# Performance work log

Hardware: AMD Instinct MI355X
Metric: run time of the kernel (lower is better)

Reference implementation:

```python
import jax, jax.numpy as jnp
import numpy as np

B, X, Y, Z = 2, 64, 64, 48
T_IN, T_OUT = 10, 20
WIDTH = 20
G = 4              # number of fields / groups
M1 = M2 = M3 = 8   # fourier modes
L = 4              # layers
ORDER = [[0, 1, 2, 3], [1, 2, 3, 0], [2, 3, 0, 1], [3, 0, 1, 2]]
CIN = WIDTH * 4    # mWidth_input_parameters[i] == 4
COUT = WIDTH       # nWidth_output_parameters[i] == 1
EPS = 1e-5


def setup_inputs() -> dict:
    key = jax.random.key(0)
    ks = jax.random.split(key, 12)
    s = 0.02
    return {
        "x": jax.random.normal(ks[0], (B, X, Y, Z, G * T_IN), jnp.float32),
        "p_w": jax.random.normal(ks[1], (G, T_IN + 3, WIDTH), jnp.float32) * s,
        "p_b": jnp.zeros((G, WIDTH), jnp.float32),
        # complex spectral weights stored as (..., 2) = (real, imag); 4 corner blocks
        "spec_w": jax.random.normal(ks[2], (L, G, 4, CIN, COUT, M1, M2, M3, 2), jnp.float32) * (1.0 / CIN),
        "mlp_w1": jax.random.normal(ks[3], (L, G, COUT, COUT), jnp.float32) * s,
        "mlp_b1": jnp.zeros((L, G, COUT), jnp.float32),
        "mlp_w2": jax.random.normal(ks[4], (L, G, COUT, COUT), jnp.float32) * s,
        "mlp_b2": jnp.zeros((L, G, COUT), jnp.float32),
        "w_w": jax.random.normal(ks[5], (L, G, COUT, CIN), jnp.float32) * s,
        "w_b": jnp.zeros((L, G, COUT), jnp.float32),
        "q_w1": jax.random.normal(ks[6], (G, 4 * COUT, COUT), jnp.float32) * s,
        "q_b1": jnp.zeros((G, 4 * COUT), jnp.float32),
        "q_w2": jax.random.normal(ks[7], (G, T_OUT, 4 * COUT), jnp.float32) * s,
        "q_b2": jnp.zeros((G, T_OUT), jnp.float32),
    }


def _instance_norm(v):  # (B,C,X,Y,Z); InstanceNorm3d, affine=False
    m = v.mean(axis=(-3, -2, -1), keepdims=True)
    var = v.var(axis=(-3, -2, -1), keepdims=True)
    return (v - m) * jax.lax.rsqrt(var + EPS)


def _conv1x1(v, w, b):  # w: (Co, Ci)
    return jnp.einsum('bixyz,oi->boxyz', v, w) + b[None, :, None, None, None]


def _gelu(v):
    return jax.nn.gelu(v, approximate=False)


def _spectral(v, w):  # v: (B,Ci,X,Y,Z); w: complex (4,Ci,Co,M1,M2,M3)
    ft = jnp.fft.rfftn(v, axes=(-3, -2, -1))
    mul = lambda xc, wc: jnp.einsum('bixyz,ioxyz->boxyz', xc, wc)
    out = jnp.zeros((v.shape[0], w.shape[2], X, Y, Z // 2 + 1), ft.dtype)
    out = out.at[:, :, :M1, :M2, :M3].set(mul(ft[:, :, :M1, :M2, :M3], w[0]))
    out = out.at[:, :, -M1:, :M2, :M3].set(mul(ft[:, :, -M1:, :M2, :M3], w[1]))
    out = out.at[:, :, :M1, -M2:, :M3].set(mul(ft[:, :, :M1, -M2:, :M3], w[2]))
    out = out.at[:, :, -M1:, -M2:, :M3].set(mul(ft[:, :, -M1:, -M2:, :M3], w[3]))
    return jnp.fft.irfftn(out, s=(X, Y, Z), axes=(-3, -2, -1))


def _grid():  # (1,X,Y,Z,3), linspace 0..1 per axis
    gx = jnp.linspace(0.0, 1.0, X, dtype=jnp.float32)[:, None, None]
    gy = jnp.linspace(0.0, 1.0, Y, dtype=jnp.float32)[None, :, None]
    gz = jnp.linspace(0.0, 1.0, Z, dtype=jnp.float32)[None, None, :]
    g = jnp.stack([jnp.broadcast_to(gx, (X, Y, Z)),
                   jnp.broadcast_to(gy, (X, Y, Z)),
                   jnp.broadcast_to(gz, (X, Y, Z))], axis=-1)
    return g[None]


def reference(x, p_w, p_b, spec_w, mlp_w1, mlp_b1, mlp_w2, mlp_b2,
              w_w, w_b, q_w1, q_b1, q_w2, q_b2):
    grid = jnp.broadcast_to(_grid(), (x.shape[0], X, Y, Z, 3))
    # --- lifting: per-field Linear(T_in+3 -> width) ---
    lifted = [jnp.concatenate([x[..., i * T_IN:(i + 1) * T_IN], grid], axis=-1) @ p_w[i] + p_b[i]
              for i in range(G)]
    h = jnp.concatenate(lifted, axis=-1).transpose(0, 4, 1, 2, 3)  # (B, width*G, X, Y, Z)
    sw = spec_w[..., 0] + 1j * spec_w[..., 1]
    for l in range(L):
        for i in range(G):
            # faithful gather quirk: first index duplicated, last index dropped
            idx = [ORDER[i][0]] + ORDER[i][:-1]
            xg = jnp.concatenate([h[:, WIDTH * k:WIDTH * (k + 1)] for k in idx], axis=1)
            v = _instance_norm(xg)
            v = _spectral(v, sw[l, i])
            v = _instance_norm(v)
            v = _conv1x1(_gelu(_conv1x1(v, mlp_w1[l, i], mlp_b1[l, i])), mlp_w2[l, i], mlp_b2[l, i])
            r = _conv1x1(xg, w_w[l, i], w_b[l, i])
            h = h.at[:, WIDTH * i:WIDTH * (i + 1)].set(v + r)
        if l != L - 1:
            h = _gelu(h)
    # --- projection: per-field MLP (T_OUT == WIDTH so slices align to field blocks) ---
    outs = []
    for i in range(G):
        lo = (WIDTH if i == 0 else T_OUT) * i
        xi = h[:, lo:lo + WIDTH]
        xi = _conv1x1(_gelu(_conv1x1(xi, q_w1[i], q_b1[i])), q_w2[i], q_b2[i])
        outs.append(xi)
    out = jnp.concatenate(outs, axis=1)
    return out.transpose(0, 2, 3, 4, 1)  # (B,X,Y,Z,G*T_OUT)
```

## Files before the change

kernel.cpp:

```cpp
#include <hip/hip_runtime.h>
#include <math.h>

#define SPAT 196608
#define EPSV 1e-5f

__device__ __forceinline__ float geluf(float x){
    return 0.5f*x*(1.0f + erff(x*0.70710678118654752440f));
}
__device__ __forceinline__ float wred(float v){
    #pragma unroll
    for(int o=32;o>0;o>>=1) v += __shfl_down(v,o);
    return v;
}

__global__ void k_tables(float* tab){
    for(int idx=threadIdx.x; idx<384; idx+=blockDim.x){
        int z = idx>>3, k = idx&7;
        double a = 6.283185307179586476925286766559 * (double)((k*z)%48) / 48.0;
        float c = (float)cos(a), s = (float)sin(a);
        tab[idx]=c; tab[384+idx]=s;
        tab[768 + k*48+z]=c; tab[1152 + k*48+z]=s;
    }
    for(int idx=threadIdx.x; idx<1024; idx+=blockDim.x){
        int y = idx>>4, ki = idx&15;
        int ka = ki<8 ? ki : ki+48;
        double a = 6.283185307179586476925286766559 * (double)((ka*y)%64) / 64.0;
        float c=(float)cos(a), s=(float)sin(a);
        tab[1536+idx]=c; tab[2560+idx]=s;
        tab[3584 + ki*64+y]=c; tab[4608 + ki*64+y]=s;
    }
}

__global__ void __launch_bounds__(256) k_lift(const float* __restrict__ x,
                       const float* __restrict__ pw, const float* __restrict__ pb,
                       float* __restrict__ h){
    int t = blockIdx.x*256 + threadIdx.x;
    int b = (t>=SPAT) ? 1 : 0; int col = t - b*SPAT;
    int xy = col/48, z = col%48;
    const float4* xp = (const float4*)(x + (size_t)t*40);
    float in[40];
    #pragma unroll
    for(int q=0;q<10;q++){
        float4 v = xp[q];
        in[q*4]=v.x; in[q*4+1]=v.y; in[q*4+2]=v.z; in[q*4+3]=v.w;
    }
    float gx = (float)(xy>>6)*(1.0f/63.0f);
    float gy = (float)(xy&63)*(1.0f/63.0f);
    float gz = (float)z*(1.0f/47.0f);
    for(int g=0;g<4;g++){
        const float* w = pw + g*260;
        #pragma unroll 4
        for(int c=0;c<20;c++){
            float a = pb[g*20+c];
            #pragma unroll
            for(int j=0;j<10;j++) a += in[g*10+j]*w[j*20+c];
            a += gx*w[200+c] + gy*w[220+c] + gz*w[240+c];
            h[(size_t)(b*80+g*20+c)*SPAT + col] = a;
        }
    }
}

__global__ void __launch_bounds__(256) k_zy(const float* __restrict__ h,
        float* __restrict__ ybuf, float* __restrict__ partZY,
        const float* __restrict__ tab, int gA,int gB,int gC,int gD){
    __shared__ __align__(16) float hl[64*52];
    __shared__ float sp[16*65];
    __shared__ float cyl[16*65], syl[16*65];
    __shared__ float sred[8];
    int blk = blockIdx.x;
    int x = blk&63; int d=(blk>>6)%20; int r2 = blk/1280; int b = r2&1; int gi = r2>>1;
    int gl4[4]={gA,gB,gC,gD};
    int g = gl4[gi];
    int ch = g*20+d;
    int tid=threadIdx.x;
    const float4* src = (const float4*)(h + (size_t)(b*80+ch)*SPAT + (size_t)x*3072);
    float s1=0,s2=0;
    #pragma unroll
    for(int u=0;u<3;u++){
        int e=tid+u*256; float4 v=src[e];
        int y=e/12, zq=e%12;
        *(float4*)(hl + y*52 + zq*4) = v;
        s1 += v.x+v.y+v.z+v.w; s2 += v.x*v.x+v.y*v.y+v.z*v.z+v.w*v.w;
    }
    for(int tt=tid;tt<1024;tt+=256){
        int ki=tt>>6, y=tt&63;
        cyl[ki*65+y]=tab[3584+tt]; syl[ki*65+y]=tab[4608+tt];
    }
    s1=wred(s1); s2=wred(s2);
    if((tid&63)==0){ sred[(tid>>6)*2]=s1; sred[(tid>>6)*2+1]=s2; }
    __syncthreads();
    if(tid==0){
        size_t pi = ((size_t)(b*80+ch)*64+x)*2;
        partZY[pi]   = sred[0]+sred[2]+sred[4]+sred[6];
        partZY[pi+1] = sred[1]+sred[3]+sred[5]+sred[7];
    }
    {
        int y = tid&63; int kq = tid>>6;
        float v[48];
        const float4* hr4 = (const float4*)(hl + y*52);
        #pragma unroll
        for(int q=0;q<12;q++){
            float4 t4=hr4[q];
            v[q*4]=t4.x; v[q*4+1]=t4.y; v[q*4+2]=t4.z; v[q*4+3]=t4.w;
        }
        #pragma unroll
        for(int kk=0;kk<2;kk++){
            int k = kq*2+kk;
            const float* CZ = tab+768+k*48;
            const float* SZ = tab+1152+k*48;
            float rr=0, si=0;
            #pragma unroll
            for(int z=0;z<48;z++){ rr += v[z]*CZ[z]; si += v[z]*SZ[z]; }
            sp[(k*2)*65+y]=rr; sp[(k*2+1)*65+y]=-si;
        }
    }
    __syncthreads();
    if(tid<128){
        int ky=tid>>3, kz=tid&7;
        const float* cy = cyl+ky*65; const float* sy = syl+ky*65;
        const float* spr = sp + (kz*2)*65;
        const float* spi = sp + (kz*2+1)*65;
        float fr=0, fi=0;
        #pragma unroll 8
        for(int y=0;y<64;y++){
            float sr=spr[y], si=spi[y];
            float c=cy[y], s=sy[y];
            fr += sr*c + si*s;
            fi += si*c - sr*s;
        }
        size_t base = ((size_t)((g*2+b)*20+d)*16 + ky)*1024 + (size_t)(kz*128);
        ybuf[base + x]      = fr;
        ybuf[base + 64 + x] = fi;
    }
}

__global__ void __launch_bounds__(128) k_xdft(const float* __restrict__ ybuf,
        float* __restrict__ fbufC, const float* __restrict__ partZY,
        const float* __restrict__ tab, int gA,int gB,int gC,int gD){
    __shared__ __align__(16) float ylx[16*68];
    __shared__ float cxl[16*65], sxl[16*65];
    __shared__ float scs[1];
    int blk = blockIdx.x;
    int kyi = blk&15; int d=(blk>>4)%20; int r2=blk/320; int b=r2&1; int gi=r2>>1;
    int gl4[4]={gA,gB,gC,gD};
    int g=gl4[gi]; int ch=g*20+d;
    int tid=threadIdx.x;
    const float4* src = (const float4*)(ybuf + (((size_t)((g*2+b)*20+d)*16+kyi)*1024));
    #pragma unroll
    for(int u=0;u<2;u++){
        int e=tid+u*128; float4 v=src[e];
        int kzri = e>>4; int xx=(e&15)*4;
        *(float4*)(ylx + kzri*68 + xx) = v;
    }
    for(int tt=tid;tt<1024;tt+=128){
        int ki=tt>>6, y=tt&63;
        cxl[ki*65+y]=tab[3584+tt]; sxl[ki*65+y]=tab[4608+tt];
    }
    float s1=0,s2=0;
    if(tid<64){
        size_t pi=((size_t)(b*80+ch)*64+tid)*2;
        s1=partZY[pi]; s2=partZY[pi+1];
    }
    s1=wred(s1); s2=wred(s2);
    if(tid==0){
        float mean=s1*(1.0f/196608.0f);
        float var=s2*(1.0f/196608.0f)-mean*mean;
        scs[0]=rsqrtf(var+EPSV);
    }
    __syncthreads();
    float sc = scs[0];
    int kxi=tid>>3, kz=tid&7;
    const float* yr = ylx + (kz*2)*68;
    const float* yi = ylx + (kz*2+1)*68;
    const float* cx = cxl + kxi*65;
    const float* sx = sxl + kxi*65;
    float fr=0, fi=0;
    #pragma unroll 8
    for(int xx=0;xx<64;xx++){
        float a=yr[xx], e2=yi[xx];
        float c=cx[xx], s=sx[xx];
        fr += a*c + e2*s;
        fi += e2*c - a*s;
    }
    fr*=sc; fi*=sc;
    if(kxi==0 && kyi==0 && kz==0){ fr=0.0f; fi=0.0f; }
    size_t idx = ((size_t)(b*80+ch)*2048 + (size_t)((kxi*16+kyi)*8+kz))*2;
    fbufC[idx]=fr; fbufC[idx+1]=fi;
}

__global__ void __launch_bounds__(256) k_spec(const float* __restrict__ fbufC,
        const float* __restrict__ sw, float* __restrict__ gbuf,
        float* __restrict__ stat2, int li, int g0, int g1, int g2){
    __shared__ float part[2112];
    int blk = blockIdx.x;
    int m1p = blk & 3, o = (blk>>2)%20, q = blk/80;
    int tid = threadIdx.x;
    int t64 = tid & 63, cc = tid >> 6;
    if(q==0 && m1p==0 && tid<2){
        stat2[(tid*20+o)*2]=0.f; stat2[(tid*20+o)*2+1]=0.f;
    }
    int offx = (q&1)*8, offy = (q>>1)*8;
    int m1 = m1p*2 + (t64>>5);
    int m2 = (t64>>2)&7;
    int m3 = (t64&3)*2;
    int tw = m1*64 + m2*8 + m3;
    int kxi = m1+offx, kyi = m2+offy;
    int fo = (kxi*16 + kyi)*8 + m3;
    const float4* wp = (const float4*)(sw + (((size_t)(li*4+q)*1600) + o)*1024 + (size_t)tw*2);
    const float4* fb = (const float4*)fbufC + (fo>>1);
    float r00=0,i00=0,r01=0,i01=0, r10=0,i10=0,r11=0,i11=0;
    int c0 = cc*5;
    #pragma unroll
    for(int u=0;u<5;u++){
        int c = c0+u;
        float4 wa = wp[(size_t)c*5120];
        float4 wb4= wp[(size_t)(c+20)*5120];
        float wr0 = wa.x + wb4.x, wi0 = wa.y + wb4.y, wr1 = wa.z + wb4.z, wi1 = wa.w + wb4.w;
        float4 f0 = fb[(size_t)(g0*20+c)*1024];
        float4 f1 = fb[(size_t)(80+g0*20+c)*1024];
        r00 += f0.x*wr0 - f0.y*wi0; i00 += f0.x*wi0 + f0.y*wr0;
        r01 += f0.z*wr1 - f0.w*wi1; i01 += f0.z*wi1 + f0.w*wr1;
        r10 += f1.x*wr0 - f1.y*wi0; i10 += f1.x*wi0 + f1.y*wr0;
        r11 += f1.z*wr1 - f1.w*wi1; i11 += f1.z*wi1 + f1.w*wr1;
    }
    #pragma unroll
    for(int u=0;u<5;u++){
        int c = c0+u;
        float4 wa = wp[(size_t)(c+40)*5120];
        float4 f0 = fb[(size_t)(g1*20+c)*1024];
        float4 f1 = fb[(size_t)(80+g1*20+c)*1024];
        r00 += f0.x*wa.x - f0.y*wa.y; i00 += f0.x*wa.y + f0.y*wa.x;
        r01 += f0.z*wa.z - f0.w*wa.w; i01 += f0.z*wa.w + f0.w*wa.z;
        r10 += f1.x*wa.x - f1.y*wa.y; i10 += f1.x*wa.y + f1.y*wa.x;
        r11 += f1.z*wa.z - f1.w*wa.w; i11 += f1.z*wa.w + f1.w*wa.z;
    }
    #pragma unroll
    for(int u=0;u<5;u++){
        int c = c0+u;
        float4 wa = wp[(size_t)(c+60)*5120];
        float4 f0 = fb[(size_t)(g2*20+c)*1024];
        float4 f1 = fb[(size_t)(80+g2*20+c)*1024];
        r00 += f0.x*wa.x - f0.y*wa.y; i00 += f0.x*wa.y + f0.y*wa.x;
        r01 += f0.z*wa.z - f0.w*wa.w; i01 += f0.z*wa.w + f0.w*wa.z;
        r10 += f1.x*wa.x - f1.y*wa.y; i10 += f1.x*wa.y + f1.y*wa.x;
        r11 += f1.z*wa.z - f1.w*wa.w; i11 += f1.z*wa.w + f1.w*wa.z;
    }
    float vals[8]={r00,i00,r01,i01,r10,i10,r11,i11};
    #pragma unroll
    for(int e=0;e<8;e++) part[t64*33 + e*4 + cc] = vals[e];
    __syncthreads();
    if(cc==0){
        float acc[8];
        #pragma unroll
        for(int e=0;e<8;e++){
            const float* p = part + t64*33 + e*4;
            acc[e] = p[0]+p[1]+p[2]+p[3];
        }
        float4* gg0 = (float4*)(gbuf + (size_t)o*4096 + fo*2);
        float4* gg1 = (float4*)(gbuf + (size_t)(20+o)*4096 + fo*2);
        *gg0 = make_float4(acc[0],acc[1],acc[2],acc[3]);
        *gg1 = make_float4(acc[4],acc[5],acc[6],acc[7]);
    }
}

__global__ void k_inv(const float* __restrict__ gbuf, float* __restrict__ iybuf,
                      float* __restrict__ stat2, const float* __restrict__ tab){
    __shared__ __align__(16) float gl[4096];
    __shared__ float tmp[256];
    __shared__ float cl[1088], sl[1088];
    __shared__ float ig[4];
    int blk = blockIdx.x;
    int nx = blk&63, o = (blk>>6)%20, b = blk/1280;
    const float4* src4 = (const float4*)(gbuf + (size_t)(b*20+o)*4096);
    for(int t=threadIdx.x;t<1024;t+=blockDim.x) ((float4*)gl)[t]=src4[t];
    for(int t=threadIdx.x;t<1024;t+=blockDim.x){
        int y=t>>4, ki=t&15;
        cl[y*17+ki]=tab[1536+t]; sl[y*17+ki]=tab[2560+t];
    }
    __syncthreads();
    {
        int kyi = threadIdx.x>>3, kz = threadIdx.x&7;
        float ar=0, ai=0;
        #pragma unroll 4
        for(int kxi=0;kxi<16;kxi++){
            float gr = gl[((kxi*16+kyi)*8+kz)*2], gi2 = gl[((kxi*16+kyi)*8+kz)*2+1];
            float c = cl[nx*17+kxi], s = sl[nx*17+kxi];
            ar += gr*c - gi2*s;
            ai += gi2*c + gr*s;
        }
        tmp[threadIdx.x*2]   = ar*(1.0f/64.0f);
        tmp[threadIdx.x*2+1] = ai*(1.0f/64.0f);
    }
    __syncthreads();
    float p1=0,p2=0;
    for(int j=0;j<4;j++){
        int out = threadIdx.x + j*128;
        int ny = out>>3, kz = out&7;
        float ar=0, ai=0;
        #pragma unroll 4
        for(int kyi=0;kyi<16;kyi++){
            float vr = tmp[(kyi*8+kz)*2], vi = tmp[(kyi*8+kz)*2+1];
            float c = cl[ny*17+kyi], s = sl[ny*17+kyi];
            ar += vr*c - vi*s;
            ai += vi*c + vr*s;
        }
        ar *= (1.0f/64.0f); ai *= (1.0f/64.0f);
        size_t idx = ((((size_t)(b*20+o)*64+nx)*64+ny)*8+kz)*2;
        iybuf[idx]=ar; iybuf[idx+1]=ai;
        if(kz==0){ p1 += ar; p2 += ar*ar; }
        else p2 += 2.0f*(ar*ar+ai*ai);
    }
    p2 *= (1.0f/48.0f);
    float r1=wred(p1), r2=wred(p2);
    int wv = threadIdx.x>>6;
    if((threadIdx.x&63)==0){ ig[wv*2]=r1; ig[wv*2+1]=r2; }
    __syncthreads();
    if(threadIdx.x==0){
        atomicAdd(&stat2[(b*20+o)*2],   ig[0]+ig[2]);
        atomicAdd(&stat2[(b*20+o)*2+1], ig[1]+ig[3]);
    }
}

__global__ void __launch_bounds__(256) k_passD(
        const float* __restrict__ iybuf,
        const float* __restrict__ w1, const float* __restrict__ b1,
        const float* __restrict__ w2, const float* __restrict__ b2,
        const float* __restrict__ ww, const float* __restrict__ wb,
        float* __restrict__ h,
        const float* __restrict__ stat2, const float* __restrict__ tab,
        int li, int grp, int g1, int g2){
    __shared__ __align__(16) float dl[2560];
    __shared__ __align__(16) float vl[20*392];
    __shared__ float m2l[20], s2l[20];
    __shared__ float czl[384], szl[384];
    int blk = blockIdx.x;
    int nyt = blk&7, nx=(blk>>3)&63, b = blk>>9;
    int tid = threadIdx.x;
    for(int u=tid; u<640; u+=256){
        int o = u>>5, j = u&31;
        const float4* s4 = (const float4*)(iybuf + ((((size_t)(b*20+o)*64+nx)*64 + nyt*8)*16));
        ((float4*)dl)[o*32+j] = s4[j];
    }
    if(tid<20){
        float S1 = stat2[(b*20+tid)*2], S2 = stat2[(b*20+tid)*2+1];
        float mean = S1*(1.0f/196608.0f);
        float var = S2*(1.0f/196608.0f) - mean*mean;
        m2l[tid]=mean; s2l[tid]=rsqrtf(var+EPSV);
    }
    for(int t=tid;t<384;t+=256){ czl[t]=tab[768+t]; szl[t]=tab[1152+t]; }
    __syncthreads();
    for(int idx=tid; idx<7680; idx+=256){
        int o = idx/384, p = idx%384;
        int ny = p/48, nz = p%48;
        const float* dd = dl + o*128 + ny*16;
        float acc = dd[0];
        #pragma unroll
        for(int k=1;k<8;k++)
            acc += 2.0f*(dd[k*2]*czl[k*48+nz] - dd[k*2+1]*szl[k*48+nz]);
        float xv = acc*(1.0f/48.0f);
        vl[o*392+p] = (xv - m2l[o])*s2l[o];
    }
    __syncthreads();
    const float* W1 = w1 + li*400;
    const float* W2 = w2 + li*400;
    const float* B1 = b1 + li*20;
    const float* B2 = b2 + li*20;
    for(int p=tid; p<384; p+=256){
        float vj[20], t1[20];
        #pragma unroll
        for(int j2=0;j2<20;j2++) vj[j2]=vl[j2*392+p];
        #pragma unroll
        for(int oo=0;oo<20;oo++){
            float a = B1[oo];
            #pragma unroll
            for(int j2=0;j2<20;j2++) a += vj[j2]*W1[oo*20+j2];
            t1[oo] = geluf(a);
        }
        #pragma unroll
        for(int oo=0;oo<20;oo++){
            float a = B2[oo];
            #pragma unroll
            for(int j2=0;j2<20;j2++) a += t1[j2]*W2[oo*20+j2];
            vl[oo*392+p] = a;
        }
    }
    __syncthreads();
    int sb = (nx*64 + nyt*8)*48;
    if(tid<192){
        const float* W = ww + li*1600;
        float2 acc[20];
        #pragma unroll
        for(int o=0;o<20;o++){ float bv = wb[li*20+o]; acc[o].x=bv; acc[o].y=bv; }
        const float* hb = h + (size_t)(b*80)*SPAT + sb + tid*2;
        for(int c=0;c<20;c++){
            float2 v = *(const float2*)(hb + (size_t)(grp*20+c)*SPAT);
            #pragma unroll
            for(int o=0;o<20;o++){
                float w = W[o*80+c] + W[o*80+20+c];
                acc[o].x += w*v.x; acc[o].y += w*v.y;
            }
        }
        for(int c=0;c<20;c++){
            float2 v = *(const float2*)(hb + (size_t)(g1*20+c)*SPAT);
            #pragma unroll
            for(int o=0;o<20;o++){
                float w = W[o*80+40+c];
                acc[o].x += w*v.x; acc[o].y += w*v.y;
            }
        }
        for(int c=0;c<20;c++){
            float2 v = *(const float2*)(hb + (size_t)(g2*20+c)*SPAT);
            #pragma unroll
            for(int o=0;o<20;o++){
                float w = W[o*80+60+c];
                acc[o].x += w*v.x; acc[o].y += w*v.y;
            }
        }
        #pragma unroll
        for(int o=0;o<20;o++){
            float2 mv = *(const float2*)(vl + o*392 + tid*2);
            float2 r; r.x = mv.x + acc[o].x; r.y = mv.y + acc[o].y;
            *(float2*)(h + (size_t)(b*80+grp*20+o)*SPAT + sb + tid*2) = r;
        }
    }
}

__global__ void k_gelu(float* __restrict__ h){
    int blk = blockIdx.x;
    size_t base = (size_t)blk*4096;
    float4* hp = (float4*)(h+base);
    for(int e=threadIdx.x;e<1024;e+=blockDim.x){
        float4 v = hp[e];
        v.x=geluf(v.x); v.y=geluf(v.y); v.z=geluf(v.z); v.w=geluf(v.w);
        hp[e]=v;
    }
}

__global__ void __launch_bounds__(256) k_head(const float* __restrict__ h,
        const float* __restrict__ qw1, const float* __restrict__ qb1,
        const float* __restrict__ qw2, const float* __restrict__ qb2,
        float* __restrict__ out){
    int g = blockIdx.x & 3;
    int t = (blockIdx.x>>2)*256 + threadIdx.x;
    if(t >= 196608) return;
    int b = (t>=98304) ? 1 : 0; int col = (t - b*98304)*2;
    const float* hb = h + (size_t)(b*80+g*20)*SPAT + col;
    float2 in20[20];
    #pragma unroll
    for(int j=0;j<20;j++) in20[j] = *(const float2*)(hb + (size_t)j*SPAT);
    float2 o20[20];
    #pragma unroll
    for(int o2=0;o2<20;o2++){ float bv = qb2[g*20+o2]; o20[o2].x=bv; o20[o2].y=bv; }
    for(int o8=0;o8<80;o8++){
        float bv = qb1[g*80+o8];
        float a0 = bv, a1 = bv;
        #pragma unroll
        for(int j=0;j<20;j++){
            float w = qw1[g*1600 + o8*20 + j];
            a0 += in20[j].x*w; a1 += in20[j].y*w;
        }
        a0 = geluf(a0); a1 = geluf(a1);
        #pragma unroll
        for(int o2=0;o2<20;o2++){
            float w = qw2[g*1600 + o2*80 + o8];
            o20[o2].x += a0*w; o20[o2].y += a1*w;
        }
    }
    float* op0 = out + ((size_t)(b*SPAT)+col)*80 + g*20;
    float* op1 = op0 + 80;
    #pragma unroll
    for(int q2=0;q2<5;q2++){
        *(float4*)(op0 + q2*4) = make_float4(o20[q2*4].x,o20[q2*4+1].x,o20[q2*4+2].x,o20[q2*4+3].x);
        *(float4*)(op1 + q2*4) = make_float4(o20[q2*4].y,o20[q2*4+1].y,o20[q2*4+2].y,o20[q2*4+3].y);
    }
}

extern "C" void kernel_launch(void* const* d_in, const int* in_sizes, int n_in,
                              void* d_out, int out_size, void* d_ws, size_t ws_size,
                              hipStream_t stream){
    (void)in_sizes; (void)n_in; (void)out_size;
    const float* x    = (const float*)d_in[0];
    const float* p_w  = (const float*)d_in[1];
    const float* p_b  = (const float*)d_in[2];
    const float* spec = (const float*)d_in[3];
    const float* w1   = (const float*)d_in[4];
    const float* b1   = (const float*)d_in[5];
    const float* w2   = (const float*)d_in[6];
    const float* b2   = (const float*)d_in[7];
    const float* ww   = (const float*)d_in[8];
    const float* wb   = (const float*)d_in[9];
    const float* qw1  = (const float*)d_in[10];
    const float* qb1  = (const float*)d_in[11];
    const float* qw2  = (const float*)d_in[12];
    const float* qb2  = (const float*)d_in[13];
    float* out = (float*)d_out;
    float* ws  = (float*)d_ws;

    if(ws_size < (size_t)37545552*4) return;

    float* h      = ws;
    float* ybuf   = ws + 31457280;
    float* gbuf   = ws + 34078720;
    float* iyb    = ws + 34242560;
    float* fbufC  = ws + 36864000;
    float* partZY = ws + 37519360;
    float* stat2  = ws + 37539840;
    float* tab    = ws + 37539920;

    k_tables<<<1,256,0,stream>>>(tab);
    k_lift<<<1536,256,0,stream>>>(x, p_w, p_b, h);

    static const int ORD3[4][3] = {{0,1,2},{1,2,3},{2,3,0},{3,0,1}};
    for(int l=0;l<4;l++){
        for(int bi=0;bi<2;bi++){
            if(bi==0){
                k_zy  <<<10240,256,0,stream>>>(h, ybuf, partZY, tab, 0,1,2,3);
                k_xdft<<< 2560,128,0,stream>>>(ybuf, fbufC, partZY, tab, 0,1,2,3);
            } else {
                k_zy  <<< 5120,256,0,stream>>>(h, ybuf, partZY, tab, 0,1,0,0);
                k_xdft<<< 1280,128,0,stream>>>(ybuf, fbufC, partZY, tab, 0,1,0,0);
            }
            for(int ii=0;ii<2;ii++){
                int i = bi*2+ii; int li = l*4+i;
                int g0=ORD3[i][0], g1=ORD3[i][1], g2=ORD3[i][2];
                (void)g0;
                k_spec <<< 320,256,0,stream>>>(fbufC, spec, gbuf, stat2, li, g0,g1,g2);
                k_inv  <<<2560,128,0,stream>>>(gbuf, iyb, stat2, tab);
                k_passD<<<1024,256,0,stream>>>(iyb, w1, b1, w2, b2, ww, wb, h, stat2, tab, li, i, g1, g2);
            }
        }
        if(l<3) k_gelu<<<7680,256,0,stream>>>(h);
    }
    k_head<<<3072,256,0,stream>>>(h, qw1, qb1, qw2, qb2, out);
}
```

Measured before the change: 3.379 ms.

## Fuse inter-layer GELU into consumers, use fast erf, and keep passD in registers

Removes the standalone GELU pass over the hidden state between layers. Instead, GELU is applied lazily wherever the not-yet-updated hidden state is read: in the z/y DFT kernel and in the residual 1x1 conv of passD, controlled by per-group flags. The z/y DFT kernel now loads its row slice straight into registers and reduces partial z-DFTs in shared memory, instead of staging the whole tile. passD computes inverse-z, the MLP and the residual conv per thread in registers, without a shared-memory round trip. GELU now uses an Abramowitz–Stegun erf polynomial with a hardware reciprocal, which trades a little accuracy for fewer instructions.

```diff
diff --git a/kernel.cpp b/kernel.cpp
--- a/kernel.cpp
+++ b/kernel.cpp
@@ -5,7 +5,12 @@
 #define EPSV 1e-5f
 
 __device__ __forceinline__ float geluf(float x){
-    return 0.5f*x*(1.0f + erff(x*0.70710678118654752440f));
+    float ax = fabsf(x)*0.70710678118654752440f;
+    float t = __builtin_amdgcn_rcpf(1.0f + 0.3275911f*ax);
+    float p = ((((1.061405429f*t - 1.453152027f)*t + 1.421413741f)*t - 0.284496736f)*t + 0.254829592f)*t;
+    float e = 1.0f - p*__expf(-ax*ax);
+    float er = copysignf(e, x);
+    return 0.5f*x*(1.0f + er);
 }
 __device__ __forceinline__ float wred(float v){
     #pragma unroll
@@ -62,9 +67,8 @@
 
 __global__ void __launch_bounds__(256) k_zy(const float* __restrict__ h,
         float* __restrict__ ybuf, float* __restrict__ partZY,
-        const float* __restrict__ tab, int gA,int gB,int gC,int gD){
-    __shared__ __align__(16) float hl[64*52];
-    __shared__ float sp[16*65];
+        const float* __restrict__ tab, int gA,int gB,int gC,int gD, int gflag){
+    __shared__ float sp4[4*16*65];
     __shared__ float cyl[16*65], syl[16*65];
     __shared__ float sred[8];
     int blk = blockIdx.x;
@@ -73,18 +77,35 @@
     int g = gl4[gi];
     int ch = g*20+d;
     int tid=threadIdx.x;
-    const float4* src = (const float4*)(h + (size_t)(b*80+ch)*SPAT + (size_t)x*3072);
+    int y = tid&63, q4 = tid>>6;
+    const float4* src = (const float4*)(h + (size_t)(b*80+ch)*SPAT + (size_t)x*3072
+                                          + (size_t)(y*48 + q4*12));
+    float v[12];
+    #pragma unroll
+    for(int u=0;u<3;u++){
+        float4 t4 = src[u];
+        v[u*4]=t4.x; v[u*4+1]=t4.y; v[u*4+2]=t4.z; v[u*4+3]=t4.w;
+    }
+    if(gflag){
+        #pragma unroll
+        for(int j=0;j<12;j++) v[j]=geluf(v[j]);
+    }
     float s1=0,s2=0;
     #pragma unroll
-    for(int u=0;u<3;u++){
-        int e=tid+u*256; float4 v=src[e];
-        int y=e/12, zq=e%12;
-        *(float4*)(hl + y*52 + zq*4) = v;
-        s1 += v.x+v.y+v.z+v.w; s2 += v.x*v.x+v.y*v.y+v.z*v.z+v.w*v.w;
-    }
+    for(int j=0;j<12;j++){ s1+=v[j]; s2+=v[j]*v[j]; }
     for(int tt=tid;tt<1024;tt+=256){
-        int ki=tt>>6, y=tt&63;
-        cyl[ki*65+y]=tab[3584+tt]; syl[ki*65+y]=tab[4608+tt];
+        int ki=tt>>6, yy=tt&63;
+        cyl[ki*65+yy]=tab[3584+tt]; syl[ki*65+yy]=tab[4608+tt];
+    }
+    const float* CZ = tab+768  + q4*12;
+    const float* SZ = tab+1152 + q4*12;
+    #pragma unroll
+    for(int k=0;k<8;k++){
+        float rr=0, si=0;
+        #pragma unroll
+        for(int j=0;j<12;j++){ rr += v[j]*CZ[k*48+j]; si += v[j]*SZ[k*48+j]; }
+        sp4[(q4*16 + k*2)*65 + y]   = rr;
+        sp4[(q4*16 + k*2+1)*65 + y] = -si;
     }
     s1=wred(s1); s2=wred(s2);
     if((tid&63)==0){ sred[(tid>>6)*2]=s1; sred[(tid>>6)*2+1]=s2; }
@@ -94,37 +115,25 @@
         partZY[pi]   = sred[0]+sred[2]+sred[4]+sred[6];
         partZY[pi+1] = sred[1]+sred[3]+sred[5]+sred[7];
     }
-    {
-        int y = tid&63; int kq = tid>>6;
-        float v[48];
-        const float4* hr4 = (const float4*)(hl + y*52);
-        #pragma unroll
-        for(int q=0;q<12;q++){
-            float4 t4=hr4[q];
-            v[q*4]=t4.x; v[q*4+1]=t4.y; v[q*4+2]=t4.z; v[q*4+3]=t4.w;
-        }
-        #pragma unroll
-        for(int kk=0;kk<2;kk++){
-            int k = kq*2+kk;
-            const float* CZ = tab+768+k*48;
-            const float* SZ = tab+1152+k*48;
-            float rr=0, si=0;
-            #pragma unroll
-            for(int z=0;z<48;z++){ rr += v[z]*CZ[z]; si += v[z]*SZ[z]; }
-            sp[(k*2)*65+y]=rr; sp[(k*2+1)*65+y]=-si;
-        }
+    #pragma unroll
+    for(int j=0;j<4;j++){
+        int e = tid + j*256;
+        int kri = e>>6, yy = e&63;
+        float sum = sp4[kri*65+yy] + sp4[(16+kri)*65+yy]
+                  + sp4[(32+kri)*65+yy] + sp4[(48+kri)*65+yy];
+        sp4[kri*65+yy] = sum;
     }
     __syncthreads();
     if(tid<128){
         int ky=tid>>3, kz=tid&7;
         const float* cy = cyl+ky*65; const float* sy = syl+ky*65;
-        const float* spr = sp + (kz*2)*65;
-        const float* spi = sp + (kz*2+1)*65;
+        const float* spr = sp4 + (kz*2)*65;
+        const float* spi = sp4 + (kz*2+1)*65;
         float fr=0, fi=0;
         #pragma unroll 8
-        for(int y=0;y<64;y++){
-            float sr=spr[y], si=spi[y];
-            float c=cy[y], s=sy[y];
+        for(int yy=0;yy<64;yy++){
+            float sr=spr[yy], si=spi[yy];
+            float c=cy[yy], s=sy[yy];
             fr += sr*c + si*s;
             fi += si*c - sr*s;
         }
@@ -328,9 +337,8 @@
         const float* __restrict__ ww, const float* __restrict__ wb,
         float* __restrict__ h,
         const float* __restrict__ stat2, const float* __restrict__ tab,
-        int li, int grp, int g1, int g2){
+        int li, int grp, int g1, int g2, int f0, int f1, int f2){
     __shared__ __align__(16) float dl[2560];
-    __shared__ __align__(16) float vl[20*392];
     __shared__ float m2l[20], s2l[20];
     __shared__ float czl[384], szl[384];
     int blk = blockIdx.x;
@@ -349,91 +357,76 @@
     }
     for(int t=tid;t<384;t+=256){ czl[t]=tab[768+t]; szl[t]=tab[1152+t]; }
     __syncthreads();
-    for(int idx=tid; idx<7680; idx+=256){
-        int o = idx/384, p = idx%384;
-        int ny = p/48, nz = p%48;
-        const float* dd = dl + o*128 + ny*16;
-        float acc = dd[0];
-        #pragma unroll
-        for(int k=1;k<8;k++)
-            acc += 2.0f*(dd[k*2]*czl[k*48+nz] - dd[k*2+1]*szl[k*48+nz]);
-        float xv = acc*(1.0f/48.0f);
-        vl[o*392+p] = (xv - m2l[o])*s2l[o];
-    }
-    __syncthreads();
-    const float* W1 = w1 + li*400;
-    const float* W2 = w2 + li*400;
-    const float* B1 = b1 + li*20;
-    const float* B2 = b2 + li*20;
-    for(int p=tid; p<384; p+=256){
-        float vj[20], t1[20];
-        #pragma unroll
-        for(int j2=0;j2<20;j2++) vj[j2]=vl[j2*392+p];
-        #pragma unroll
-        for(int oo=0;oo<20;oo++){
-            float a = B1[oo];
-            #pragma unroll
-            for(int j2=0;j2<20;j2++) a += vj[j2]*W1[oo*20+j2];
-            t1[oo] = geluf(a);
-        }
-        #pragma unroll
-        for(int oo=0;oo<20;oo++){
-            float a = B2[oo];
-            #pragma unroll
-            for(int j2=0;j2<20;j2++) a += t1[j2]*W2[oo*20+j2];
-            vl[oo*392+p] = a;
-        }
-    }
-    __syncthreads();
+    if(tid>=192) return;
+    int p0 = tid*2;
+    int nyl = p0/48, nz0 = p0 - nyl*48;
+    float vj0[20], vj1[20];
+    #pragma unroll
+    for(int o=0;o<20;o++){
+        const float* dd = dl + o*128 + nyl*16;
+        float a0 = dd[0], a1 = dd[0];
+        #pragma unroll
+        for(int k=1;k<8;k++){
+            float dr = dd[k*2], di = dd[k*2+1];
+            a0 += 2.0f*(dr*czl[k*48+nz0]   - di*szl[k*48+nz0]);
+            a1 += 2.0f*(dr*czl[k*48+nz0+1] - di*szl[k*48+nz0+1]);
+        }
+        vj0[o] = (a0*(1.0f/48.0f) - m2l[o])*s2l[o];
+        vj1[o] = (a1*(1.0f/48.0f) - m2l[o])*s2l[o];
+    }
+    const float* W1 = w1 + li*400; const float* W2 = w2 + li*400;
+    const float* B1 = b1 + li*20;  const float* B2 = b2 + li*20;
+    float t10[20], t11[20];
+    #pragma unroll
+    for(int oo=0;oo<20;oo++){
+        float a0=B1[oo], a1=a0;
+        #pragma unroll
+        for(int j=0;j<20;j++){ float w=W1[oo*20+j]; a0+=vj0[j]*w; a1+=vj1[j]*w; }
+        t10[oo]=geluf(a0); t11[oo]=geluf(a1);
+    }
+    float o0[20], o1[20];
+    #pragma unroll
+    for(int oo=0;oo<20;oo++){
+        float a0=B2[oo], a1=a0;
+        #pragma unroll
+        for(int j=0;j<20;j++){ float w=W2[oo*20+j]; a0+=t10[j]*w; a1+=t11[j]*w; }
+        o0[oo]=a0; o1[oo]=a1;
+    }
     int sb = (nx*64 + nyt*8)*48;
-    if(tid<192){
-        const float* W = ww + li*1600;
-        float2 acc[20];
-        #pragma unroll
-        for(int o=0;o<20;o++){ float bv = wb[li*20+o]; acc[o].x=bv; acc[o].y=bv; }
-        const float* hb = h + (size_t)(b*80)*SPAT + sb + tid*2;
-        for(int c=0;c<20;c++){
-            float2 v = *(const float2*)(hb + (size_t)(grp*20+c)*SPAT);
-            #pragma unroll
-            for(int o=0;o<20;o++){
-                float w = W[o*80+c] + W[o*80+20+c];
-                acc[o].x += w*v.x; acc[o].y += w*v.y;
-            }
-        }
-        for(int c=0;c<20;c++){
-            float2 v = *(const float2*)(hb + (size_t)(g1*20+c)*SPAT);
-            #pragma unroll
-            for(int o=0;o<20;o++){
-                float w = W[o*80+40+c];
-                acc[o].x += w*v.x; acc[o].y += w*v.y;
-            }
-        }
-        for(int c=0;c<20;c++){
-            float2 v = *(const float2*)(hb + (size_t)(g2*20+c)*SPAT);
-            #pragma unroll
-            for(int o=0;o<20;o++){
-                float w = W[o*80+60+c];
-                acc[o].x += w*v.x; acc[o].y += w*v.y;
-            }
-        }
+    const float* W = ww + li*1600;
+    const float* hb = h + (size_t)(b*80)*SPAT + sb + p0;
+    #pragma unroll
+    for(int o=0;o<20;o++){ float bv=wb[li*20+o]; o0[o]+=bv; o1[o]+=bv; }
+    for(int c=0;c<20;c++){
+        float2 vv = *(const float2*)(hb + (size_t)(grp*20+c)*SPAT);
+        if(f0){ vv.x=geluf(vv.x); vv.y=geluf(vv.y); }
         #pragma unroll
         for(int o=0;o<20;o++){
-            float2 mv = *(const float2*)(vl + o*392 + tid*2);
-            float2 r; r.x = mv.x + acc[o].x; r.y = mv.y + acc[o].y;
-            *(float2*)(h + (size_t)(b*80+grp*20+o)*SPAT + sb + tid*2) = r;
-        }
-    }
-}
-
-__global__ void k_gelu(float* __restrict__ h){
-    int blk = blockIdx.x;
-    size_t base = (size_t)blk*4096;
-    float4* hp = (float4*)(h+base);
-    for(int e=threadIdx.x;e<1024;e+=blockDim.x){
-        float4 v = hp[e];
-        v.x=geluf(v.x); v.y=geluf(v.y); v.z=geluf(v.z); v.w=geluf(v.w);
-        hp[e]=v;
-    }
+            float w = W[o*80+c] + W[o*80+20+c];
+            o0[o]+=w*vv.x; o1[o]+=w*vv.y;
+        }
+    }
+    for(int c=0;c<20;c++){
+        float2 vv = *(const float2*)(hb + (size_t)(g1*20+c)*SPAT);
+        if(f1){ vv.x=geluf(vv.x); vv.y=geluf(vv.y); }
+        #pragma unroll
+        for(int o=0;o<20;o++){
+            float w = W[o*80+40+c];
+            o0[o]+=w*vv.x; o1[o]+=w*vv.y;
+        }
+    }
+    for(int c=0;c<20;c++){
+        float2 vv = *(const float2*)(hb + (size_t)(g2*20+c)*SPAT);
+        if(f2){ vv.x=geluf(vv.x); vv.y=geluf(vv.y); }
+        #pragma unroll
+        for(int o=0;o<20;o++){
+            float w = W[o*80+60+c];
+            o0[o]+=w*vv.x; o1[o]+=w*vv.y;
+        }
+    }
+    #pragma unroll
+    for(int o=0;o<20;o++)
+        *(float2*)(h + (size_t)(b*80+grp*20+o)*SPAT + sb + p0) = make_float2(o0[o],o1[o]);
 }
 
 __global__ void __launch_bounds__(256) k_head(const float* __restrict__ h,
@@ -512,24 +505,28 @@
 
     static const int ORD3[4][3] = {{0,1,2},{1,2,3},{2,3,0},{3,0,1}};
     for(int l=0;l<4;l++){
+        int lf = (l>0)?1:0;
         for(int bi=0;bi<2;bi++){
             if(bi==0){
-                k_zy  <<<10240,256,0,stream>>>(h, ybuf, partZY, tab, 0,1,2,3);
+                k_zy  <<<10240,256,0,stream>>>(h, ybuf, partZY, tab, 0,1,2,3, lf);
                 k_xdft<<< 2560,128,0,stream>>>(ybuf, fbufC, partZY, tab, 0,1,2,3);
             } else {
-                k_zy  <<< 5120,256,0,stream>>>(h, ybuf, partZY, tab, 0,1,0,0);
+                k_zy  <<< 5120,256,0,stream>>>(h, ybuf, partZY, tab, 0,1,0,0, 0);
                 k_xdft<<< 1280,128,0,stream>>>(ybuf, fbufC, partZY, tab, 0,1,0,0);
             }
             for(int ii=0;ii<2;ii++){
                 int i = bi*2+ii; int li = l*4+i;
                 int g0=ORD3[i][0], g1=ORD3[i][1], g2=ORD3[i][2];
                 (void)g0;
-                k_spec <<< 320,256,0,stream>>>(fbufC, spec, gbuf, stat2, li, g0,g1,g2);
+                int f0 = lf;
+                int f1 = (g1<i)?0:lf;
+                int f2 = (g2<i)?0:lf;
+                k_spec <<< 320,256,0,stream>>>(fbufC, spec, gbuf, stat2, li, i, g1, g2);
                 k_inv  <<<2560,128,0,stream>>>(gbuf, iyb, stat2, tab);
-                k_passD<<<1024,256,0,stream>>>(iyb, w1, b1, w2, b2, ww, wb, h, stat2, tab, li, i, g1, g2);
+                k_passD<<<1024,256,0,stream>>>(iyb, w1, b1, w2, b2, ww, wb, h, stat2, tab,
+                                               li, i, g1, g2, f0, f1, f2);
             }
         }
-        if(l<3) k_gelu<<<7680,256,0,stream>>>(h);
     }
     k_head<<<3072,256,0,stream>>>(h, qw1, qb1, qw2, qb2, out);
 }
```

Measured after the change: 3.269 ms. 1.03x faster.
